# Kernel optimization log

Hardware: AMD Instinct MI355X
Metric: run time of the kernel (lower is better)

Reference implementation:

```python
import jax, jax.numpy as jnp
import numpy as np
import math

B, S, D, K = 8, 2048, 1024, 64
EPS = 1e-5

def _ln(x):
    m = jnp.mean(x, axis=-1, keepdims=True)
    v = jnp.mean((x - m) ** 2, axis=-1, keepdims=True)
    return (x - m) * jax.lax.rsqrt(v + EPS)

def setup_inputs() -> dict:
    key = jax.random.key(0)
    ks = jax.random.split(key, 14)
    s = 0.02
    return {
        "x":  jax.random.normal(ks[0], (B, S, D), dtype=jnp.float32),
        "Wk": jax.random.normal(ks[1], (D, K), dtype=jnp.float32) * s,
        "bk": jnp.zeros((K,), dtype=jnp.float32),
        "Wq": jax.random.normal(ks[2], (D, K), dtype=jnp.float32) * s,
        "bq": jnp.zeros((K,), dtype=jnp.float32),
        "Wv": jax.random.normal(ks[3], (D, D), dtype=jnp.float32) * s,
        "bv": jnp.zeros((D,), dtype=jnp.float32),
        "Wb": jax.random.normal(ks[4], (D, 1), dtype=jnp.float32) * s,
        "bb": jnp.zeros((1,), dtype=jnp.float32),
        "W1": jax.random.normal(ks[5], (D, D), dtype=jnp.float32) * s,
        "b1": jnp.zeros((D,), dtype=jnp.float32),
        "g1": jnp.ones((D,), dtype=jnp.float32),
        "be1": jnp.zeros((D,), dtype=jnp.float32),
    }

def reference(x, Wk, bk, Wq, bq, Wv, bv, Wb, bb, W1, b1, g1, be1):
    scale = 1.0 / math.sqrt(K)
    keys    = (jnp.einsum('bsd,dk->bsk', x, Wk) + bk) * scale   # [B,S,K]
    queries = jnp.einsum('bsd,dk->bsk', x, Wq) + bq             # [B,S,K]
    values  = jnp.einsum('bsd,de->bse', x, Wv) + bv             # [B,S,D]
    biases  = jnp.einsum('bsd,do->bso', x, Wb) + bb             # [B,S,1]
    # scores[b,i,j] = keys[b,i] . queries[b,j] + biases[b,i]
    scores = jax.nn.sigmoid(jnp.einsum('bik,bjk->bij', keys, queries) + biases)
    attention = jnp.einsum('bij,bjd->bid', scores, values)      # [B,S,D]
    res = _ln(x + attention) * g1 + be1
    feedforward = jax.nn.relu(jnp.einsum('bsd,de->bse', res, W1) + b1)
    return _ln(res + feedforward)
```

## Files before the change

kernel.cpp:

```cpp
#include <hip/hip_runtime.h>
#include <math.h>


typedef __bf16 bf16_t;
typedef __bf16 bf16x4_t __attribute__((ext_vector_type(4)));
typedef __bf16 bf16x8_t __attribute__((ext_vector_type(8)));
typedef float  f32x4    __attribute__((ext_vector_type(4)));

#define DEV static __device__ __forceinline__

DEV void gll16(const void* g, void* l) {
  __builtin_amdgcn_global_load_lds(
      (const __attribute__((address_space(1))) void*)g,
      (__attribute__((address_space(3))) void*)l, 16, 0, 0);
}

template <int MODE, int MFAST>
__global__ __launch_bounds__(512, 2) void gemm256(
    const bf16_t* __restrict__ A, const bf16_t* __restrict__ B,
    bf16_t* __restrict__ C, int K, int lda, int ldb, int ldc,
    long sAb, long sBb, long sCb, const float* __restrict__ aux0) {
  const int gx = gridDim.x, gy = gridDim.y;
  const int gxy = gx * gy;
  const int nwg = gxy * (int)gridDim.z;
  const int orig = blockIdx.x + gx * blockIdx.y + gxy * blockIdx.z;
  const int lid = (orig & 7) * (nwg >> 3) + (orig >> 3);
  const int bz = lid / gxy;
  const int rem = lid - bz * gxy;
  const int bx = MFAST ? (rem / gy) : (rem % gx);
  const int by = MFAST ? (rem % gy) : (rem / gx);

  A += (long)bz * sAb;
  B += (long)bz * sBb;
  const int m0 = by * 256, n0 = bx * 256;

  __shared__ bf16_t SM[65536];
#define ASH(b, h) (&SM[(((b)*2 + (h)) << 13)])
#define BSH(b, h) (&SM[32768 + (((b)*2 + (h)) << 13)])

  const int tid = threadIdx.x;
  const int wid = tid >> 6, l = tid & 63;
  const int wr = wid >> 2, wc = wid & 3;
  const int lr = l & 15, lh = l >> 4;

  const int sRow = tid >> 2;
  const int sSl = (tid & 3) ^ ((tid >> 3) & 3);
  const bf16_t* Asrc = A + (long)(m0 + sRow) * lda + sSl * 8;
  const bf16_t* Bsrc = B + (long)(n0 + sRow) * ldb + sSl * 8;
  const long aStep = (long)128 * lda, bStep = (long)128 * ldb;

#define STAGE_A(b, h, kt) do { \
    const bf16_t* s_ = Asrc + (kt) * 64 + (h) * 32; \
    gll16(s_,         ASH(b, h) + tid * 8); \
    gll16(s_ + aStep, ASH(b, h) + 4096 + tid * 8); } while (0)
#define STAGE_B(b, h, kt) do { \
    const bf16_t* s_ = Bsrc + (kt) * 64 + (h) * 32; \
    gll16(s_,         BSH(b, h) + tid * 8); \
    gll16(s_ + bStep, BSH(b, h) + 4096 + tid * 8); } while (0)

  const int sw = (lh ^ ((lr >> 1) & 3)) * 8;
  const int aOff = (wr * 128 + lr) * 32 + sw;
  const int bOff = (wc * 64 + lr) * 32 + sw;

  f32x4 acc[8][4] = {};
  const int NT = K >> 6;

  STAGE_A(0, 0, 0); STAGE_B(0, 0, 0); STAGE_A(0, 1, 0); STAGE_B(0, 1, 0);
  asm volatile("s_waitcnt vmcnt(4)" ::: "memory");
  __builtin_amdgcn_s_barrier();

#define PHASE_SYNC() do { \
    __builtin_amdgcn_sched_barrier(0); \
    __builtin_amdgcn_s_barrier(); \
    asm volatile("s_waitcnt lgkmcnt(0)" ::: "memory"); \
    __builtin_amdgcn_sched_barrier(0); } while (0)
#define MFMA_LO() do { \
    __builtin_amdgcn_s_setprio(1); \
    _Pragma("unroll") for (int m = 0; m < 4; ++m) \
    _Pragma("unroll") for (int n = 0; n < 4; ++n) \
      acc[m][n] = __builtin_amdgcn_mfma_f32_16x16x32_bf16(aF[m], bF[n], acc[m][n], 0, 0, 0); \
    __builtin_amdgcn_s_setprio(0); } while (0)
#define MFMA_HI() do { \
    __builtin_amdgcn_s_setprio(1); \
    _Pragma("unroll") for (int m = 0; m < 4; ++m) \
    _Pragma("unroll") for (int n = 0; n < 4; ++n) \
      acc[m + 4][n] = __builtin_amdgcn_mfma_f32_16x16x32_bf16(aG[m], bF[n], acc[m + 4][n], 0, 0, 0); \
    __builtin_amdgcn_s_setprio(0); } while (0)

  for (int t = 0; t < NT; ++t) {
    const int p = t & 1, q = p ^ 1;
    const bool pf = (t + 1 < NT);
    bf16x8_t bF[4], aF[4], aG[4];

#pragma unroll
    for (int n = 0; n < 4; ++n) bF[n] = *(const bf16x8_t*)(BSH(p, 0) + bOff + n * 512);
#pragma unroll
    for (int m = 0; m < 4; ++m) aF[m] = *(const bf16x8_t*)(ASH(p, 0) + aOff + m * 512);
    if (pf) STAGE_A(q, 0, t + 1);
    PHASE_SYNC();
    MFMA_LO();

#pragma unroll
    for (int m = 0; m < 4; ++m) aG[m] = *(const bf16x8_t*)(ASH(p, 0) + aOff + (m + 4) * 512);
    if (pf) {
      STAGE_B(q, 0, t + 1);
      asm volatile("s_waitcnt vmcnt(4)" ::: "memory");
    } else {
      asm volatile("s_waitcnt vmcnt(0)" ::: "memory");
    }
    PHASE_SYNC();
    MFMA_HI();

#pragma unroll
    for (int n = 0; n < 4; ++n) bF[n] = *(const bf16x8_t*)(BSH(p, 1) + bOff + n * 512);
#pragma unroll
    for (int m = 0; m < 4; ++m) aF[m] = *(const bf16x8_t*)(ASH(p, 1) + aOff + m * 512);
    if (pf) STAGE_A(q, 1, t + 1);
    PHASE_SYNC();
    MFMA_LO();

#pragma unroll
    for (int m = 0; m < 4; ++m) aG[m] = *(const bf16x8_t*)(ASH(p, 1) + aOff + (m + 4) * 512);
    if (pf) STAGE_B(q, 1, t + 1);
    asm volatile("s_waitcnt vmcnt(4)" ::: "memory");
    PHASE_SYNC();
    MFMA_HI();
  }
#undef STAGE_A
#undef STAGE_B
#undef PHASE_SYNC
#undef MFMA_LO
#undef MFMA_HI

  bf16_t* Cb = C + (long)bz * sCb;
  const int rowb = m0 + wr * 128 + lh * 4;
  const int colb = n0 + wc * 64 + lr;
#pragma unroll
  for (int m = 0; m < 8; ++m)
#pragma unroll
    for (int n = 0; n < 4; ++n) {
      const f32x4 v = acc[m][n];
      const int cc = colb + n * 16;
#pragma unroll
      for (int r = 0; r < 4; ++r) {
        const int rr = rowb + m * 16 + r;
        const float val = v[r];
        if constexpr (MODE == 1) {
          Cb[(long)rr * ldc + cc] = (bf16_t)(val + aux0[rr]);
        } else if constexpr (MODE == 3) {
          Cb[(long)rr * ldc + cc] = (bf16_t)val;
        } else {
          Cb[(long)rr * ldc + cc] = (bf16_t)fmaxf(val + aux0[cc], 0.0f);
        }
      }
    }
#undef ASH
#undef BSH
}

__global__ __launch_bounds__(256) void kq_thin(
    const bf16_t* __restrict__ A, const bf16_t* __restrict__ B,
    bf16_t* __restrict__ C,
    const float* __restrict__ bk, const float* __restrict__ bq) {
  const int m0 = blockIdx.x * 64;

  __shared__ bf16_t SM[12288];
#define ASH(b) (&SM[(b) << 11])
#define BSH(b) (&SM[4096 + ((b) << 12)])

  const int tid = threadIdx.x;
  const int w = tid >> 6, l = tid & 63;
  const int lr = l & 15, lh = l >> 4;

  const int sRow = tid >> 2;
  const int sSl = (tid & 3) ^ ((tid >> 3) & 3);
  const bf16_t* Asrc = A + (long)(m0 + sRow) * 1024 + sSl * 8;
  const bf16_t* Bsrc0 = B + (long)sRow * 1024 + sSl * 8;
  const bf16_t* Bsrc1 = B + (long)(64 + sRow) * 1024 + sSl * 8;

  const int sw = (lh ^ ((lr >> 1) & 3)) * 8;
  const int aOff = (w * 16 + lr) * 32 + sw;

  f32x4 acc[8] = {};

  auto stage = [&](int buf, int k0) {
    gll16(Asrc + k0, ASH(buf) + tid * 8);
    gll16(Bsrc0 + k0, BSH(buf) + tid * 8);
    gll16(Bsrc1 + k0, BSH(buf) + 2048 + tid * 8);
  };

  stage(0, 0);
  __syncthreads();
  int cur = 0;

  for (int k0 = 0; k0 < 1024; k0 += 32) {
    if (k0 + 32 < 1024) stage(cur ^ 1, k0 + 32);

    const bf16x8_t aF = *(const bf16x8_t*)(ASH(cur) + aOff);
    bf16x8_t bF[8];
#pragma unroll
    for (int j = 0; j < 8; ++j)
      bF[j] = *(const bf16x8_t*)(BSH(cur) + (j * 16 + lr) * 32 + sw);
#pragma unroll
    for (int j = 0; j < 8; ++j)
      acc[j] = __builtin_amdgcn_mfma_f32_16x16x32_bf16(aF, bF[j], acc[j], 0, 0, 0);

    __syncthreads();
    cur ^= 1;
  }

  {
#pragma unroll
    for (int j = 0; j < 8; ++j) {
      const f32x4 v = acc[j];
      const int cl = j * 16 + lr;
      const float b = (cl < 64) ? bk[cl] : bq[cl - 64];
      const float s = (cl < 64) ? 0.125f : 1.0f;
#pragma unroll
      for (int r = 0; r < 4; ++r) {
        const int rl = w * 16 + lh * 4 + r;
        SM[rl * 128 + (cl ^ (lh << 4))] = (bf16_t)((v[r] + b) * s);
      }
    }
    __syncthreads();
    const int chunk = tid & 15, rsub = tid >> 4;
#pragma unroll
    for (int pp = 0; pp < 4; ++pp) {
      const int rl = pp * 16 + rsub;
      const int sc = chunk ^ (((rl >> 2) & 3) << 1);
      const bf16x8_t vv = *(const bf16x8_t*)&SM[rl * 128 + sc * 8];
      *(bf16x8_t*)&C[(long)(m0 + rl) * 128 + chunk * 8] = vv;
    }
  }
#undef ASH
#undef BSH
}

template <int MODE, int MFAST>
__global__ __launch_bounds__(256) void gemm_bt(
    const bf16_t* __restrict__ A, const bf16_t* __restrict__ B,
    void* __restrict__ Cv, int M, int N, int K, int lda, int ldb, int ldc,
    long sAb, long sBb, long sCb,
    const float* __restrict__ aux0, const float* __restrict__ aux1, long sAux) {
  const int gx = gridDim.x, gy = gridDim.y;
  const int gxy = gx * gy;
  const int nwg = gxy * (int)gridDim.z;
  const int orig = blockIdx.x + gx * blockIdx.y + gxy * blockIdx.z;
  const int q = nwg >> 3, r8 = nwg & 7;
  const int xcd = orig & 7, seq = orig >> 3;
  const int lid = (xcd < r8 ? xcd * (q + 1) : r8 * (q + 1) + (xcd - r8) * q) + seq;
  const int bz = lid / gxy;
  const int rem = lid - bz * gxy;
  const int bx = MFAST ? (rem / gy) : (rem % gx);
  const int by = MFAST ? (rem % gy) : (rem / gx);

  A += (long)bz * sAb;
  B += (long)bz * sBb;
  const float* a0 = (MODE == 2) ? (aux0 + (long)bz * sAux) : aux0;

  const int m0 = by * 128;
  const int n0 = bx * 128;

  __shared__ bf16_t SM[16384];
#define ASH(b) (&SM[(b) << 12])
#define BSH(b) (&SM[8192 + ((b) << 12)])

  const int tid = threadIdx.x;
  const int w = tid >> 6, l = tid & 63;
  const int wr = w >> 1, wc = w & 1;
  const int lr = l & 15, lh = l >> 4;

  const int srow = l >> 2;
  const int scol = (((l & 3) ^ (srow & 3)) << 3);

  f32x4 acc[4][4] = {};

  auto stage = [&](int buf, int k0) {
#pragma unroll
    for (int half = 0; half < 2; ++half) {
      const int i = 2 * w + half;
      const int row = (i << 4) + srow;
      gll16(A + (long)(m0 + row) * lda + k0 + scol, ASH(buf) + (i << 9));
      gll16(B + (long)(n0 + row) * ldb + k0 + scol, BSH(buf) + (i << 9));
    }
  };

  stage(0, 0);
  __syncthreads();
  int cur = 0;
  const int sw = ((lh ^ (lr & 3)) << 3);

  for (int k0 = 0; k0 < K; k0 += 32) {
    if (k0 + 32 < K) stage(cur ^ 1, k0 + 32);

    bf16x8_t af[4], bfm[4];
#pragma unroll
    for (int m = 0; m < 4; ++m)
      af[m] = *(const bf16x8_t*)(ASH(cur) + (((wr << 6) + (m << 4) + lr) << 5) + sw);
#pragma unroll
    for (int n = 0; n < 4; ++n)
      bfm[n] = *(const bf16x8_t*)(BSH(cur) + (((wc << 6) + (n << 4) + lr) << 5) + sw);
#pragma unroll
    for (int m = 0; m < 4; ++m)
#pragma unroll
      for (int n = 0; n < 4; ++n)
        acc[m][n] = __builtin_amdgcn_mfma_f32_16x16x32_bf16(af[m], bfm[n], acc[m][n], 0, 0, 0);

    __syncthreads();
    cur ^= 1;
  }

  {
    const int rowb = (wr << 6) + (lh << 2);
    const int colb = (wc << 6) + lr;
#pragma unroll
    for (int m = 0; m < 4; ++m)
#pragma unroll
      for (int n = 0; n < 4; ++n) {
        const f32x4 v = acc[m][n];
        const int cl = colb + (n << 4);
#pragma unroll
        for (int r = 0; r < 4; ++r) {
          const int rl = rowb + (m << 4) + r;
          const float zz = v[r] + a0[m0 + rl];
          SM[rl * 128 + (cl ^ (lh << 4))] =
              (bf16_t)__builtin_amdgcn_rcpf(1.0f + __expf(-zz));
        }
      }
    __syncthreads();
    bf16_t* Cb = (bf16_t*)Cv + (long)bz * sCb;
    const int chunk = tid & 15, rsub = tid >> 4;
#pragma unroll
    for (int pp = 0; pp < 8; ++pp) {
      const int rl = pp * 16 + rsub;
      const int sc = chunk ^ (((rl >> 2) & 3) << 1);
      const bf16x8_t vv = *(const bf16x8_t*)&SM[rl * 128 + sc * 8];
      *(bf16x8_t*)&Cb[(long)(m0 + rl) * ldc + n0 + chunk * 8] = vv;
    }
  }
#undef ASH
#undef BSH
}

__global__ __launch_bounds__(256) void cast_bias_kernel(
    const float* __restrict__ x, const float* __restrict__ Wb,
    const float* __restrict__ bb, bf16_t* __restrict__ x_bf,
    float* __restrict__ biases) {
  const int r = blockIdx.x * 4 + (threadIdx.x >> 6);
  const int l = threadIdx.x & 63;
  const float* xr = x + (long)r * 1024;
  bf16_t* orow = x_bf + (long)r * 1024;
  float s = 0.f;
#pragma unroll
  for (int i = 0; i < 4; ++i) {
    const int off = l * 4 + i * 256;
    const float4 v = *(const float4*)(xr + off);
    const float4 w = *(const float4*)(Wb + off);
    s += v.x * w.x + v.y * w.y + v.z * w.z + v.w * w.w;
    bf16x4_t o;
    o[0] = (bf16_t)v.x; o[1] = (bf16_t)v.y; o[2] = (bf16_t)v.z; o[3] = (bf16_t)v.w;
    *(bf16x4_t*)(orow + off) = o;
  }
#pragma unroll
  for (int off = 1; off < 64; off <<= 1) s += __shfl_xor(s, off);
  if (l == 0) biases[r] = s + bb[0];
}

__global__ __launch_bounds__(256) void transpose_cast_kernel(
    const float* __restrict__ in, bf16_t* __restrict__ out, int R, int C) {
  __shared__ float t[32][33];
  const int c0 = blockIdx.x * 32, r0 = blockIdx.y * 32;
  const int tx = threadIdx.x & 31, ty = threadIdx.x >> 5;
#pragma unroll
  for (int i = 0; i < 4; ++i) {
    const int rl = ty * 4 + i;
    t[rl][tx] = in[(long)(r0 + rl) * C + c0 + tx];
  }
  __syncthreads();
#pragma unroll
  for (int i = 0; i < 4; ++i) {
    const int rl = ty * 4 + i;
    out[(long)(c0 + rl) * R + r0 + tx] = (bf16_t)t[tx][rl];
  }
}

DEV float2 block_sum2(float s, float ss) {
#pragma unroll
  for (int off = 1; off < 64; off <<= 1) {
    s += __shfl_xor(s, off);
    ss += __shfl_xor(ss, off);
  }
  __shared__ float bs[4], bss[4];
  const int w = threadIdx.x >> 6, l = threadIdx.x & 63;
  if (l == 0) { bs[w] = s; bss[w] = ss; }
  __syncthreads();
  s = bs[0] + bs[1] + bs[2] + bs[3];
  ss = bss[0] + bss[1] + bss[2] + bss[3];
  return make_float2(s, ss);
}

__global__ __launch_bounds__(256) void ln1_kernel(
    const bf16_t* __restrict__ x, const bf16_t* __restrict__ attn,
    const float* __restrict__ g, const float* __restrict__ be,
    bf16_t* __restrict__ res) {
  const long r = blockIdx.x;
  const int t = threadIdx.x;
  const bf16x4_t xv = *(const bf16x4_t*)(x + r * 1024 + t * 4);
  const bf16x4_t av = *(const bf16x4_t*)(attn + r * 1024 + t * 4);
  const float y0 = (float)xv[0] + (float)av[0], y1 = (float)xv[1] + (float)av[1];
  const float y2 = (float)xv[2] + (float)av[2], y3 = (float)xv[3] + (float)av[3];
  const float2 s2 = block_sum2(y0 + y1 + y2 + y3, y0 * y0 + y1 * y1 + y2 * y2 + y3 * y3);
  const float mean = s2.x * (1.0f / 1024.0f);
  const float var = s2.y * (1.0f / 1024.0f) - mean * mean;
  const float rs = rsqrtf(var + 1e-5f);
  const int c = t * 4;
  bf16x4_t o;
  o[0] = (bf16_t)((y0 - mean) * rs * g[c + 0] + be[c + 0]);
  o[1] = (bf16_t)((y1 - mean) * rs * g[c + 1] + be[c + 1]);
  o[2] = (bf16_t)((y2 - mean) * rs * g[c + 2] + be[c + 2]);
  o[3] = (bf16_t)((y3 - mean) * rs * g[c + 3] + be[c + 3]);
  *(bf16x4_t*)(res + r * 1024 + c) = o;
}

__global__ __launch_bounds__(256) void ln2_kernel(
    const bf16_t* __restrict__ res, const bf16_t* __restrict__ h,
    float* __restrict__ out) {
  const long r = blockIdx.x;
  const int t = threadIdx.x;
  const bf16x4_t rv = *(const bf16x4_t*)(res + r * 1024 + t * 4);
  const bf16x4_t hv = *(const bf16x4_t*)(h + r * 1024 + t * 4);
  const float y0 = (float)rv[0] + (float)hv[0], y1 = (float)rv[1] + (float)hv[1];
  const float y2 = (float)rv[2] + (float)hv[2], y3 = (float)rv[3] + (float)hv[3];
  const float2 s2 = block_sum2(y0 + y1 + y2 + y3, y0 * y0 + y1 * y1 + y2 * y2 + y3 * y3);
  const float mean = s2.x * (1.0f / 1024.0f);
  const float var = s2.y * (1.0f / 1024.0f) - mean * mean;
  const float rs = rsqrtf(var + 1e-5f);
  float4 o;
  o.x = (y0 - mean) * rs; o.y = (y1 - mean) * rs;
  o.z = (y2 - mean) * rs; o.w = (y3 - mean) * rs;
  ((float4*)(out + r * 1024))[t] = o;
}

extern "C" void kernel_launch(void* const* d_in, const int* in_sizes, int n_in,
                              void* d_out, int out_size, void* d_ws, size_t ws_size,
                              hipStream_t stream) {
  const float* x   = (const float*)d_in[0];
  const float* Wk  = (const float*)d_in[1];
  const float* bk  = (const float*)d_in[2];
  const float* Wq  = (const float*)d_in[3];
  const float* bq  = (const float*)d_in[4];
  const float* Wv  = (const float*)d_in[5];
  const float* bv  = (const float*)d_in[6];
  const float* Wb  = (const float*)d_in[7];
  const float* bb  = (const float*)d_in[8];
  const float* W1  = (const float*)d_in[9];
  const float* b1  = (const float*)d_in[10];
  const float* g1  = (const float*)d_in[11];
  const float* be1 = (const float*)d_in[12];
  float* out = (float*)d_out;

  char* ws = (char*)d_ws;
  bf16_t* x_bf    = (bf16_t*)(ws + 0);
  bf16_t* vt_bf   = (bf16_t*)(ws + 33554432);
  bf16_t* kq_bf   = (bf16_t*)(ws + 67108864);
  bf16_t* Wkqt    = (bf16_t*)(ws + 71303168);
  bf16_t* Wvt     = (bf16_t*)(ws + 71565312);
  bf16_t* W1t     = (bf16_t*)(ws + 73662464);
  float*  biases  = (float*) (ws + 75759616);
  bf16_t* scores  = (bf16_t*)(ws + 75825152);
  bf16_t* attn_bf = (bf16_t*)(ws + 142934016);
  bf16_t* res_bf  = (bf16_t*)(ws + 176488448);
  bf16_t* h_bf    = attn_bf;

  cast_bias_kernel<<<4096, 256, 0, stream>>>(x, Wb, bb, x_bf, biases);
  transpose_cast_kernel<<<dim3(2, 32), 256, 0, stream>>>(Wk, Wkqt, 1024, 64);
  transpose_cast_kernel<<<dim3(2, 32), 256, 0, stream>>>(Wq, Wkqt + 64 * 1024, 1024, 64);
  transpose_cast_kernel<<<dim3(32, 32), 256, 0, stream>>>(Wv, Wvt, 1024, 1024);
  transpose_cast_kernel<<<dim3(32, 32), 256, 0, stream>>>(W1, W1t, 1024, 1024);

  kq_thin<<<256, 256, 0, stream>>>(x_bf, Wkqt, kq_bf, bk, bq);

  gemm256<1, 1><<<dim3(64, 4, 1), 512, 0, stream>>>(
      Wvt, x_bf, vt_bf, 1024, 1024, 1024, 16384, 0, 0, 0, bv);

  gemm_bt<2, 0><<<dim3(16, 16, 8), 256, 0, stream>>>(
      kq_bf, kq_bf + 64, scores, 2048, 2048, 64, 128, 128, 2048,
      2048L * 128, 2048L * 128, 2048L * 2048, biases, nullptr, 2048);

  gemm256<3, 0><<<dim3(4, 8, 8), 512, 0, stream>>>(
      scores, vt_bf, attn_bf, 2048, 2048, 16384, 1024,
      2048L * 2048, 2048, 2048L * 1024, nullptr);

  ln1_kernel<<<16384, 256, 0, stream>>>(x_bf, attn_bf, g1, be1, res_bf);

  gemm256<4, 0><<<dim3(4, 64, 1), 512, 0, stream>>>(
      res_bf, W1t, h_bf, 1024, 1024, 1024, 1024, 0, 0, 0, b1);

  ln2_kernel<<<16384, 256, 0, stream>>>(res_bf, h_bf, out);
}
```

Measured before the change: 241.6 us.

## Add pipelined 256-tile GEMM for attention and wave-per-row layernorms

Adds a new gemm256p kernel for the scores×values GEMM. It uses a 128KB LDS double-buffered schedule with half-K stages, interleaving global-to-LDS loads, LDS reads and MFMA issue under explicit waitcnt/barrier control and setprio, to overlap memory with compute. It also rewrites both layernorm kernels so one wavefront handles one row with 16-byte vector loads and pure shuffle reductions. This removes the shared-memory block reduction and __syncthreads, at the cost of 4x fewer blocks. The large LDS footprint limits occupancy, and the hand-tuned waitcnt counts risk races if miscounted.

```diff
diff --git a/kernel.cpp b/kernel.cpp
--- a/kernel.cpp
+++ b/kernel.cpp
@@ -147,11 +147,150 @@
         const float val = v[r];
         if constexpr (MODE == 1) {
           Cb[(long)rr * ldc + cc] = (bf16_t)(val + aux0[rr]);
-        } else if constexpr (MODE == 3) {
-          Cb[(long)rr * ldc + cc] = (bf16_t)val;
         } else {
           Cb[(long)rr * ldc + cc] = (bf16_t)fmaxf(val + aux0[cc], 0.0f);
         }
+      }
+    }
+#undef ASH
+#undef BSH
+}
+
+template <int MODE>
+__global__ __launch_bounds__(512, 2) void gemm256p(
+    const bf16_t* __restrict__ A, const bf16_t* __restrict__ B,
+    bf16_t* __restrict__ C, int K, int lda, int ldb, int ldc,
+    long sAb, long sBb, long sCb, const float* __restrict__ aux0) {
+  const int gx = gridDim.x, gy = gridDim.y;
+  const int gxy = gx * gy;
+  const int nwg = gxy * (int)gridDim.z;
+  const int orig = blockIdx.x + gx * blockIdx.y + gxy * blockIdx.z;
+  const int lid = (orig & 7) * (nwg >> 3) + (orig >> 3);
+  const int bz = lid / gxy;
+  const int rem = lid - bz * gxy;
+  const int bx = rem % gx;
+  const int by = rem / gx;
+
+  A += (long)bz * sAb;
+  B += (long)bz * sBb;
+  const int m0 = by * 256, n0 = bx * 256;
+
+  __shared__ bf16_t SM[65536];
+#define ASH(b, h) (&SM[(((b)*2 + (h)) << 13)])
+#define BSH(b, h) (&SM[32768 + (((b)*2 + (h)) << 13)])
+
+  const int tid = threadIdx.x;
+  const int wid = tid >> 6, l = tid & 63;
+  const int wr = wid >> 2, wc = wid & 3;
+  const int lr = l & 15, lh = l >> 4;
+
+  const int sRow = tid >> 2;
+  const int sSl = (tid & 3) ^ ((tid >> 3) & 3);
+  const bf16_t* Asrc = A + (long)(m0 + sRow) * lda + sSl * 8;
+  const bf16_t* Bsrc = B + (long)(n0 + sRow) * ldb + sSl * 8;
+  const long aStep = (long)128 * lda, bStep = (long)128 * ldb;
+
+#define STAGE_A(b, h, kt) do { \
+    const bf16_t* s_ = Asrc + (kt) * 64 + (h) * 32; \
+    gll16(s_,         ASH(b, h) + tid * 8); \
+    gll16(s_ + aStep, ASH(b, h) + 4096 + tid * 8); } while (0)
+#define STAGE_B(b, h, kt) do { \
+    const bf16_t* s_ = Bsrc + (kt) * 64 + (h) * 32; \
+    gll16(s_,         BSH(b, h) + tid * 8); \
+    gll16(s_ + bStep, BSH(b, h) + 4096 + tid * 8); } while (0)
+
+  const int sw = (lh ^ ((lr >> 1) & 3)) * 8;
+  const int aOff = (wr * 128 + lr) * 32 + sw;
+  const int bOff = (wc * 64 + lr) * 32 + sw;
+
+  f32x4 acc[8][4] = {};
+  const int NT = K >> 6;
+
+#define LGKM(n) do { \
+    asm volatile("s_waitcnt lgkmcnt(" #n ")" ::: "memory"); \
+    __builtin_amdgcn_sched_barrier(0); } while (0)
+#define MFMA16(AS, BS, mo) do { \
+    __builtin_amdgcn_s_setprio(1); \
+    _Pragma("unroll") for (int m = 0; m < 4; ++m) \
+    _Pragma("unroll") for (int n = 0; n < 4; ++n) \
+      acc[m + (mo)][n] = __builtin_amdgcn_mfma_f32_16x16x32_bf16(AS[m], BS[n], acc[m + (mo)][n], 0, 0, 0); \
+    __builtin_amdgcn_s_setprio(0); } while (0)
+
+  STAGE_A(0, 0, 0); STAGE_B(0, 0, 0); STAGE_A(0, 1, 0); STAGE_B(0, 1, 0);
+  asm volatile("s_waitcnt vmcnt(4)" ::: "memory");
+  __builtin_amdgcn_s_barrier();
+
+  bf16x8_t aA[4], aB[4], bA[4], bB[4];
+#pragma unroll
+  for (int n = 0; n < 4; ++n) bA[n] = *(const bf16x8_t*)(BSH(0, 0) + bOff + n * 512);
+#pragma unroll
+  for (int m = 0; m < 4; ++m) aA[m] = *(const bf16x8_t*)(ASH(0, 0) + aOff + m * 512);
+
+  for (int t = 0; t < NT; ++t) {
+    const int p = t & 1, q = p ^ 1;
+    const bool pf = (t + 1 < NT);
+
+#pragma unroll
+    for (int m = 0; m < 4; ++m) aB[m] = *(const bf16x8_t*)(ASH(p, 0) + aOff + (m + 4) * 512);
+    if (pf) STAGE_A(q, 0, t + 1);
+    LGKM(4);
+    MFMA16(aA, bA, 0);
+
+    if (pf) {
+      asm volatile("s_waitcnt vmcnt(2)" ::: "memory");
+    } else {
+      asm volatile("s_waitcnt vmcnt(0)" ::: "memory");
+    }
+    __builtin_amdgcn_sched_barrier(0);
+    __builtin_amdgcn_s_barrier();
+#pragma unroll
+    for (int m = 0; m < 4; ++m) aA[m] = *(const bf16x8_t*)(ASH(p, 1) + aOff + m * 512);
+#pragma unroll
+    for (int n = 0; n < 4; ++n) bB[n] = *(const bf16x8_t*)(BSH(p, 1) + bOff + n * 512);
+    if (pf) STAGE_B(q, 0, t + 1);
+    LGKM(8);
+    MFMA16(aB, bA, 4);
+
+#pragma unroll
+    for (int m = 0; m < 4; ++m) aB[m] = *(const bf16x8_t*)(ASH(p, 1) + aOff + (m + 4) * 512);
+    if (pf) STAGE_A(q, 1, t + 1);
+    LGKM(4);
+    MFMA16(aA, bB, 0);
+
+    if (pf) STAGE_B(q, 1, t + 1);
+    asm volatile("s_waitcnt lgkmcnt(0)" ::: "memory");
+    if (pf) {
+      asm volatile("s_waitcnt vmcnt(4)" ::: "memory");
+    }
+    __builtin_amdgcn_sched_barrier(0);
+    __builtin_amdgcn_s_barrier();
+    if (pf) {
+#pragma unroll
+      for (int n = 0; n < 4; ++n) bA[n] = *(const bf16x8_t*)(BSH(q, 0) + bOff + n * 512);
+#pragma unroll
+      for (int m = 0; m < 4; ++m) aA[m] = *(const bf16x8_t*)(ASH(q, 0) + aOff + m * 512);
+    }
+    __builtin_amdgcn_sched_barrier(0);
+    MFMA16(aB, bB, 4);
+  }
+#undef STAGE_A
+#undef STAGE_B
+#undef LGKM
+#undef MFMA16
+
+  bf16_t* Cb = C + (long)bz * sCb;
+  const int rowb = m0 + wr * 128 + lh * 4;
+  const int colb = n0 + wc * 64 + lr;
+#pragma unroll
+  for (int m = 0; m < 8; ++m)
+#pragma unroll
+    for (int n = 0; n < 4; ++n) {
+      const f32x4 v = acc[m][n];
+      const int cc = colb + n * 16;
+#pragma unroll
+      for (int r = 0; r < 4; ++r) {
+        const int rr = rowb + m * 16 + r;
+        Cb[(long)rr * ldc + cc] = (bf16_t)v[r];
       }
     }
 #undef ASH
@@ -256,7 +395,7 @@
 
   A += (long)bz * sAb;
   B += (long)bz * sBb;
-  const float* a0 = (MODE == 2) ? (aux0 + (long)bz * sAux) : aux0;
+  const float* a0 = aux0 + (long)bz * sAux;
 
   const int m0 = by * 128;
   const int n0 = bx * 128;
@@ -384,61 +523,87 @@
   }
 }
 
-DEV float2 block_sum2(float s, float ss) {
-#pragma unroll
-  for (int off = 1; off < 64; off <<= 1) {
-    s += __shfl_xor(s, off);
-    ss += __shfl_xor(ss, off);
-  }
-  __shared__ float bs[4], bss[4];
-  const int w = threadIdx.x >> 6, l = threadIdx.x & 63;
-  if (l == 0) { bs[w] = s; bss[w] = ss; }
-  __syncthreads();
-  s = bs[0] + bs[1] + bs[2] + bs[3];
-  ss = bss[0] + bss[1] + bss[2] + bss[3];
-  return make_float2(s, ss);
-}
-
 __global__ __launch_bounds__(256) void ln1_kernel(
     const bf16_t* __restrict__ x, const bf16_t* __restrict__ attn,
     const float* __restrict__ g, const float* __restrict__ be,
     bf16_t* __restrict__ res) {
-  const long r = blockIdx.x;
-  const int t = threadIdx.x;
-  const bf16x4_t xv = *(const bf16x4_t*)(x + r * 1024 + t * 4);
-  const bf16x4_t av = *(const bf16x4_t*)(attn + r * 1024 + t * 4);
-  const float y0 = (float)xv[0] + (float)av[0], y1 = (float)xv[1] + (float)av[1];
-  const float y2 = (float)xv[2] + (float)av[2], y3 = (float)xv[3] + (float)av[3];
-  const float2 s2 = block_sum2(y0 + y1 + y2 + y3, y0 * y0 + y1 * y1 + y2 * y2 + y3 * y3);
-  const float mean = s2.x * (1.0f / 1024.0f);
-  const float var = s2.y * (1.0f / 1024.0f) - mean * mean;
-  const float rs = rsqrtf(var + 1e-5f);
-  const int c = t * 4;
-  bf16x4_t o;
-  o[0] = (bf16_t)((y0 - mean) * rs * g[c + 0] + be[c + 0]);
-  o[1] = (bf16_t)((y1 - mean) * rs * g[c + 1] + be[c + 1]);
-  o[2] = (bf16_t)((y2 - mean) * rs * g[c + 2] + be[c + 2]);
-  o[3] = (bf16_t)((y3 - mean) * rs * g[c + 3] + be[c + 3]);
-  *(bf16x4_t*)(res + r * 1024 + c) = o;
+  const int w = threadIdx.x >> 6, l = threadIdx.x & 63;
+  const long r = (long)blockIdx.x * 4 + w;
+  const bf16_t* xr = x + r * 1024;
+  const bf16_t* ar = attn + r * 1024;
+  float y[16];
+  float s = 0.f, ss = 0.f;
+#pragma unroll
+  for (int h = 0; h < 2; ++h) {
+    const int base = h * 512 + l * 8;
+    const bf16x8_t xv = *(const bf16x8_t*)(xr + base);
+    const bf16x8_t av = *(const bf16x8_t*)(ar + base);
+#pragma unroll
+    for (int j = 0; j < 8; ++j) {
+      const float yy = (float)xv[j] + (float)av[j];
+      y[h * 8 + j] = yy;
+      s += yy; ss += yy * yy;
+    }
+  }
+#pragma unroll
+  for (int off = 1; off < 64; off <<= 1) {
+    s += __shfl_xor(s, off);
+    ss += __shfl_xor(ss, off);
+  }
+  const float mean = s * (1.0f / 1024.0f);
+  const float rs = rsqrtf(ss * (1.0f / 1024.0f) - mean * mean + 1e-5f);
+  bf16_t* orow = res + r * 1024;
+#pragma unroll
+  for (int h = 0; h < 2; ++h) {
+    const int base = h * 512 + l * 8;
+    bf16x8_t o;
+#pragma unroll
+    for (int j = 0; j < 8; ++j)
+      o[j] = (bf16_t)((y[h * 8 + j] - mean) * rs * g[base + j] + be[base + j]);
+    *(bf16x8_t*)(orow + base) = o;
+  }
 }
 
 __global__ __launch_bounds__(256) void ln2_kernel(
-    const bf16_t* __restrict__ res, const bf16_t* __restrict__ h,
+    const bf16_t* __restrict__ res, const bf16_t* __restrict__ hh,
     float* __restrict__ out) {
-  const long r = blockIdx.x;
-  const int t = threadIdx.x;
-  const bf16x4_t rv = *(const bf16x4_t*)(res + r * 1024 + t * 4);
-  const bf16x4_t hv = *(const bf16x4_t*)(h + r * 1024 + t * 4);
-  const float y0 = (float)rv[0] + (float)hv[0], y1 = (float)rv[1] + (float)hv[1];
-  const float y2 = (float)rv[2] + (float)hv[2], y3 = (float)rv[3] + (float)hv[3];
-  const float2 s2 = block_sum2(y0 + y1 + y2 + y3, y0 * y0 + y1 * y1 + y2 * y2 + y3 * y3);
-  const float mean = s2.x * (1.0f / 1024.0f);
-  const float var = s2.y * (1.0f / 1024.0f) - mean * mean;
-  const float rs = rsqrtf(var + 1e-5f);
-  float4 o;
-  o.x = (y0 - mean) * rs; o.y = (y1 - mean) * rs;
-  o.z = (y2 - mean) * rs; o.w = (y3 - mean) * rs;
-  ((float4*)(out + r * 1024))[t] = o;
+  const int w = threadIdx.x >> 6, l = threadIdx.x & 63;
+  const long r = (long)blockIdx.x * 4 + w;
+  const bf16_t* rr = res + r * 1024;
+  const bf16_t* hr = hh + r * 1024;
+  float y[16];
+  float s = 0.f, ss = 0.f;
+#pragma unroll
+  for (int h = 0; h < 2; ++h) {
+    const int base = h * 512 + l * 8;
+    const bf16x8_t rv = *(const bf16x8_t*)(rr + base);
+    const bf16x8_t hv = *(const bf16x8_t*)(hr + base);
+#pragma unroll
+    for (int j = 0; j < 8; ++j) {
+      const float yy = (float)rv[j] + (float)hv[j];
+      y[h * 8 + j] = yy;
+      s += yy; ss += yy * yy;
+    }
+  }
+#pragma unroll
+  for (int off = 1; off < 64; off <<= 1) {
+    s += __shfl_xor(s, off);
+    ss += __shfl_xor(ss, off);
+  }
+  const float mean = s * (1.0f / 1024.0f);
+  const float rs = rsqrtf(ss * (1.0f / 1024.0f) - mean * mean + 1e-5f);
+  float* orow = out + r * 1024;
+#pragma unroll
+  for (int h = 0; h < 2; ++h) {
+    const int base = h * 512 + l * 8;
+    float4 o1, o2;
+    o1.x = (y[h * 8 + 0] - mean) * rs; o1.y = (y[h * 8 + 1] - mean) * rs;
+    o1.z = (y[h * 8 + 2] - mean) * rs; o1.w = (y[h * 8 + 3] - mean) * rs;
+    o2.x = (y[h * 8 + 4] - mean) * rs; o2.y = (y[h * 8 + 5] - mean) * rs;
+    o2.z = (y[h * 8 + 6] - mean) * rs; o2.w = (y[h * 8 + 7] - mean) * rs;
+    *(float4*)(orow + base) = o1;
+    *(float4*)(orow + base + 4) = o2;
+  }
 }
 
 extern "C" void kernel_launch(void* const* d_in, const int* in_sizes, int n_in,
@@ -487,14 +652,14 @@
       kq_bf, kq_bf + 64, scores, 2048, 2048, 64, 128, 128, 2048,
       2048L * 128, 2048L * 128, 2048L * 2048, biases, nullptr, 2048);
 
-  gemm256<3, 0><<<dim3(4, 8, 8), 512, 0, stream>>>(
+  gemm256p<3><<<dim3(4, 8, 8), 512, 0, stream>>>(
       scores, vt_bf, attn_bf, 2048, 2048, 16384, 1024,
       2048L * 2048, 2048, 2048L * 1024, nullptr);
 
-  ln1_kernel<<<16384, 256, 0, stream>>>(x_bf, attn_bf, g1, be1, res_bf);
+  ln1_kernel<<<4096, 256, 0, stream>>>(x_bf, attn_bf, g1, be1, res_bf);
 
   gemm256<4, 0><<<dim3(4, 64, 1), 512, 0, stream>>>(
       res_bf, W1t, h_bf, 1024, 1024, 1024, 1024, 0, 0, 0, b1);
 
-  ln2_kernel<<<16384, 256, 0, stream>>>(res_bf, h_bf, out);
-}
+  ln2_kernel<<<4096, 256, 0, stream>>>(res_bf, h_bf, out);
+}
```

Measured after the change: 240.9 us. Within noise of the previous version (-0.3%).
